# Kernel tuning notes

Measured on AMD Instinct MI355X. Metric: run time of the kernel, lower is better.

The kernel has to match this reference:

```python
import jax, jax.numpy as jnp
import numpy as np

MARGIN = 1.0
BATCH = 512
NFEAT = 128
NTRIP = 1024


def setup_inputs() -> dict:
    key = jax.random.key(0)
    k1, k2 = jax.random.split(key)
    embeddings = jax.random.normal(k1, (BATCH, NFEAT), dtype=jnp.float32)
    triplets = jax.random.randint(k2, (NTRIP, 3), 0, BATCH, dtype=jnp.int64)
    return {"embeddings": embeddings, "triplets": triplets}


def _triplet_loss(embeddings, triplets, margin):
    pivot = embeddings[triplets[:, 0]]
    positives = embeddings[triplets[:, 1]]
    negatives = embeddings[triplets[:, 2]]
    ap = jnp.sum((pivot - positives) ** 2, axis=1)
    an = jnp.sum((pivot - negatives) ** 2, axis=1)
    return jnp.mean(jax.nn.relu(ap - an + margin))


def _dist_corr_loss(embeddings):
    # embeddings: [B, n]; treat each feature column as a 1-D sample.
    B, n = embeddings.shape
    X = embeddings.T  # [n, B]
    # Per-column pairwise L1 distance matrices: [n, B, B]
    D = jnp.abs(X[:, :, None] - X[:, None, :])
    m = jnp.mean(D, axis=1)                      # [n, B] row/col means (D symmetric)
    g = jnp.mean(m, axis=1)                      # [n] grand means
    A = D - m[:, None, :] - m[:, :, None] + g[:, None, None]  # double-centered
    # S[i, j] = mean(A_i * A_j) over the B*B entries
    S = jnp.einsum('iab,jab->ij', A, A) / (B * B)
    diag = jnp.diagonal(S)                       # mean(A_i^2) = varA_i^2 pre-sqrt
    # dCov(i,j) = sqrt(S_ij); dCorr = dCov / sqrt(sqrt(S_ii)*sqrt(S_jj))
    denom = jnp.sqrt(jnp.sqrt(diag)[:, None] * jnp.sqrt(diag)[None, :])
    corr = jnp.sqrt(S) / denom                   # [n, n]
    iu, ju = jnp.triu_indices(n, k=1)
    return jnp.mean(corr[iu, ju])


def reference(embeddings, triplets):
    triplet_loss = _triplet_loss(embeddings, triplets, MARGIN)
    corr_loss = _dist_corr_loss(embeddings)
    return triplet_loss + corr_loss
```

## Files before the change

kernel.cpp:

```cpp
#include <hip/hip_runtime.h>
#include <hip/hip_bf16.h>

#define B_    512
#define F_    128
#define NTRIP 1024
#define MARGIN 1.0f
#define NBLK  32
#define NPAIRB 132
#define NFOLD  4
#define PREP  130

#define OFF_M    0
#define OFF_MT   65536
#define OFF_G    131072
#define OFF_TL   131200
#define OFF_SQ   131216
#define OFF_PART 147600

typedef __attribute__((ext_vector_type(8))) short bf16x8;
typedef __attribute__((ext_vector_type(4))) float f32x4;

#define LDS_ROW 20

__device__ inline unsigned int bf16r(float f) {
    unsigned int u = __float_as_uint(f);
    u += 0x7FFFu + ((u >> 16) & 1u);
    return u >> 16;
}

__global__ __launch_bounds__(512)
void k1_prep_pair(const float* __restrict__ emb, const int* __restrict__ trip,
                  float* __restrict__ m, float* __restrict__ mT,
                  float* __restrict__ g, float* __restrict__ tl,
                  float* __restrict__ sq, float* __restrict__ out,
                  unsigned short* __restrict__ part) {
    __shared__ __align__(16) unsigned int dt[4 * F_ * LDS_ROW];
    const int bid = blockIdx.x;
    const int t   = threadIdx.x;

    if (bid >= NPAIRB) {
        const int pbb = bid - NPAIRB;
        if (pbb < F_) {
            float*  x    = (float*)dt;
            float4* red4 = (float4*)((float*)dt + 512);
            const int i = pbb;
            if (i == 0 && t == 0) out[0] = 0.f;
            x[t] = emb[t * F_ + i];
            __syncthreads();
            const float xav = x[t];
            float s0 = 0.f, s1 = 0.f, s2 = 0.f, s3 = 0.f;
            for (int b = 0; b < B_; b += 4) {
                s0 += fabsf(xav - x[b]);
                s1 += fabsf(xav - x[b + 1]);
                s2 += fabsf(xav - x[b + 2]);
                s3 += fabsf(xav - x[b + 3]);
            }
            float s = (s0 + s1) + (s2 + s3);
            float mv = s * (1.f / B_);
            m[i * B_ + t]  = mv;
            mT[t * F_ + i] = mv;
            red4[t] = make_float4(s, xav, xav * xav, mv * mv);
            __syncthreads();
            for (int sh = 256; sh > 0; sh >>= 1) {
                if (t < sh) {
                    float4 a = red4[t], b = red4[t + sh];
                    red4[t] = make_float4(a.x + b.x, a.y + b.y, a.z + b.z, a.w + b.w);
                }
                __syncthreads();
            }
            if (t == 0) {
                float4 r = red4[0];
                const float Bf = (float)B_;
                float gi = r.x * (1.f / (Bf * Bf));
                g[i] = gi;
                float DD  = 2.f * Bf * r.z - 2.f * r.y * r.y;
                float Sii = DD * (1.f / (Bf * Bf)) - (2.f / Bf) * r.w + gi * gi;
                sq[i] = sqrtf(sqrtf(fmaxf(Sii, 0.f)));
            }
        } else {
            float* red = (float*)dt;
            const int tt = (pbb - F_) * 512 + t;
            int a = trip[3 * tt]     & (B_ - 1);
            int p = trip[3 * tt + 1] & (B_ - 1);
            int n = trip[3 * tt + 2] & (B_ - 1);
            const float4* ea = (const float4*)(emb + a * F_);
            const float4* ep = (const float4*)(emb + p * F_);
            const float4* en = (const float4*)(emb + n * F_);
            float ap = 0.f, an = 0.f;
            #pragma unroll 8
            for (int f4 = 0; f4 < F_ / 4; ++f4) {
                float4 va = ea[f4], vp = ep[f4], vn = en[f4];
                float d;
                d = va.x - vp.x; ap = fmaf(d, d, ap);
                d = va.y - vp.y; ap = fmaf(d, d, ap);
                d = va.z - vp.z; ap = fmaf(d, d, ap);
                d = va.w - vp.w; ap = fmaf(d, d, ap);
                d = va.x - vn.x; an = fmaf(d, d, an);
                d = va.y - vn.y; an = fmaf(d, d, an);
                d = va.z - vn.z; an = fmaf(d, d, an);
                d = va.w - vn.w; an = fmaf(d, d, an);
            }
            float l = fmaxf(ap - an + MARGIN, 0.f);
            red[t] = l;
            __syncthreads();
            for (int sh = 256; sh > 0; sh >>= 1) {
                if (t < sh) red[t] += red[t + sh];
                __syncthreads();
            }
            if (t == 0) tl[pbb - F_] = red[0];
        }
        return;
    }

    const int pbp = bid;
    const int lane = t & 63;
    const int w    = t >> 6;
    const int wr   = w >> 1;
    const int wc   = w & 1;
    const int i    = t & 127;
    const int pg   = t >> 7;
    const int fr_row = lane & 15;
    const int fr_k4  = (lane >> 4) * 4;

    int baA[NFOLD], bbA[NFOLD];
    #pragma unroll
    for (int u = 0; u < NFOLD; ++u) {
        int L = pbp + u * NPAIRB;
        int ba = 0, rem = L;
        while (rem >= NBLK - ba) { rem -= NBLK - ba; ++ba; }
        baA[u] = ba; bbA[u] = ba + rem;
    }

    f32x4 acc[2][4];
    #pragma unroll
    for (int q = 0; q < 2; ++q)
        #pragma unroll
        for (int c = 0; c < 4; ++c) acc[q][c] = (f32x4)(0.f);

    float xb[2][16], xa[2][4];
    #pragma unroll
    for (int b = 0; b < 16; ++b) xb[0][b] = emb[(bbA[0] * 16 + b) * F_ + i];
    #pragma unroll
    for (int k = 0; k < 4; ++k)
        xa[0][k] = emb[(baA[0] * 16 + (k >> 1) * 8 + pg * 2 + (k & 1)) * F_ + i];

    #pragma unroll
    for (int u = 0; u < NFOLD; ++u) {
        const int cu = u & 1, nx = cu ^ 1;
        const bool diag = (baA[u] == bbA[u]);
        #pragma unroll
        for (int h = 0; h < 2; ++h) {
            if (h | u) __syncthreads();
            #pragma unroll
            for (int ar2 = 0; ar2 < 2; ++ar2) {
                const float xav = xa[cu][h * 2 + ar2];
                const int pa = h * 8 + pg * 2 + ar2;
                unsigned int pk[8];
                #pragma unroll
                for (int q = 0; q < 8; ++q) {
                    float d0 = fabsf(xav - xb[cu][2 * q]);
                    float d1 = fabsf(xav - xb[cu][2 * q + 1]);
                    if (diag && pa >= 2 * q)     d0 = 0.f;
                    if (diag && pa >= 2 * q + 1) d1 = 0.f;
                    pk[q] = bf16r(d0) | (bf16r(d1) << 16);
                }
                unsigned int* dst = &dt[pg * (F_ * LDS_ROW) + i * LDS_ROW + ar2 * 8];
                *reinterpret_cast<uint4*>(dst)     = make_uint4(pk[0], pk[1], pk[2], pk[3]);
                *reinterpret_cast<uint4*>(dst + 4) = make_uint4(pk[4], pk[5], pk[6], pk[7]);
            }
            if (h == 1 && u < NFOLD - 1) {
                #pragma unroll
                for (int b = 0; b < 16; ++b)
                    xb[nx][b] = emb[(bbA[u + 1] * 16 + b) * F_ + i];
                #pragma unroll
                for (int k = 0; k < 4; ++k)
                    xa[nx][k] = emb[(baA[u + 1] * 16 + (k >> 1) * 8 + pg * 2 + (k & 1)) * F_ + i];
            }
            __syncthreads();
            #pragma unroll
            for (int c = 0; c < 4; ++c) {
                const unsigned int* base = &dt[c * (F_ * LDS_ROW)];
                const bf16x8 fA0 = *reinterpret_cast<const bf16x8*>(
                    &base[((wr * 2 + 0) * 16 + fr_row) * LDS_ROW + fr_k4]);
                const bf16x8 fA1 = *reinterpret_cast<const bf16x8*>(
                    &base[((wr * 2 + 1) * 16 + fr_row) * LDS_ROW + fr_k4]);
                #pragma unroll
                for (int cg = 0; cg < 4; ++cg) {
                    const bf16x8 fB = *reinterpret_cast<const bf16x8*>(
                        &base[((wc * 4 + cg) * 16 + fr_row) * LDS_ROW + fr_k4]);
                    acc[0][cg] = __builtin_amdgcn_mfma_f32_16x16x32_bf16(fA0, fB, acc[0][cg], 0, 0, 0);
                    acc[1][cg] = __builtin_amdgcn_mfma_f32_16x16x32_bf16(fA1, fB, acc[1][cg], 0, 0, 0);
                }
            }
        }
    }

    unsigned short* dstp = part + (size_t)pbp * (F_ * F_);
    const int cj = lane & 15;
    const int rsub = (lane >> 4) * 4;
    #pragma unroll
    for (int q = 0; q < 2; ++q)
        #pragma unroll
        for (int cg = 0; cg < 4; ++cg)
            #pragma unroll
            for (int r = 0; r < 4; ++r)
                dstp[((wr * 2 + q) * 16 + rsub + r) * F_ + (wc * 4 + cg) * 16 + cj] =
                    (unsigned short)bf16r(acc[q][cg][r]);
}

__global__ __launch_bounds__(512)
void k2_srow_final(const unsigned short* __restrict__ part,
                   const float* __restrict__ m, const float* __restrict__ mT,
                   const float* __restrict__ g, const float* __restrict__ sq,
                   const float* __restrict__ tl, float* __restrict__ out) {
    __shared__ float shT[16][64];
    __shared__ float shM[8][64];
    __shared__ float smi[B_];
    __shared__ float red[64];
    const int bid = blockIdx.x;
    const int i   = bid >> 1;
    const int jh  = bid & 1;
    const int t   = threadIdx.x;

    const int dw = t & 31;
    const int sl = t >> 5;
    const unsigned int* src = reinterpret_cast<const unsigned int*>(part)
                            + i * 64 + jh * 32 + dw;
    float tlo = 0.f, thi = 0.f;
    #pragma unroll
    for (int k = 0; k < 9; ++k) {
        const int s = sl + 16 * k;
        if (s < NPAIRB) {
            unsigned int v = src[(size_t)s * 8192];
            tlo += __uint_as_float(v << 16);
            thi += __uint_as_float(v & 0xFFFF0000u);
        }
    }
    shT[sl][dw * 2]     = tlo;
    shT[sl][dw * 2 + 1] = thi;
    smi[t] = m[i * B_ + t];
    __syncthreads();

    const int jl = t & 63;
    const int j  = jh * 64 + jl;
    const int q8 = t >> 6;
    float md = 0.f;
    const float* mta = mT + (size_t)(q8 * 64) * F_ + j;
    const float* mia = smi + q8 * 64;
    #pragma unroll 8
    for (int a = 0; a < 64; ++a) md = fmaf(mia[a], mta[(size_t)a * F_], md);
    shM[q8][jl] = md;
    __syncthreads();

    if (t < 64) {
        float T = 0.f;
        #pragma unroll
        for (int s = 0; s < 16; ++s) T += shT[s][t];
        float mdj = 0.f;
        #pragma unroll
        for (int s = 0; s < 8; ++s) mdj += shM[s][t];
        const int jj = jh * 64 + t;
        float Sij = 2.f * T * (1.f / ((float)B_ * (float)B_))
                  - (2.f / (float)B_) * mdj
                  + g[i] * g[jj];
        float c = 0.f;
        if (jj > i) c = sqrtf(fmaxf(Sij, 0.f)) / (sq[i] * sq[jj]);
        red[t] = c;
    }
    __syncthreads();
    for (int sh = 32; sh > 0; sh >>= 1) {
        if (t < sh) red[t] += red[t + sh];
        __syncthreads();
    }
    if (t == 0) {
        float v = red[0] * (1.f / 8128.f);
        if (bid == 0) v += (tl[0] + tl[1]) * (1.f / (float)NTRIP);
        atomicAdd(out, v);
    }
}

extern "C" void kernel_launch(void* const* d_in, const int* in_sizes, int n_in,
                              void* d_out, int out_size, void* d_ws, size_t ws_size,
                              hipStream_t stream) {
    const float* emb = (const float*)d_in[0];
    const int*   trp = (const int*)d_in[1];
    float* ws  = (float*)d_ws;
    float* m   = ws + OFF_M;
    float* mT  = ws + OFF_MT;
    float* g   = ws + OFF_G;
    float* tl  = ws + OFF_TL;
    float* sq  = ws + OFF_SQ;
    unsigned short* part = (unsigned short*)(ws + OFF_PART);
    float* out = (float*)d_out;

    k1_prep_pair  <<<NPAIRB + PREP, 512, 0, stream>>>(emb, trp, m, mT, g, tl, sq, out, part);
    k2_srow_final <<<256, 512, 0, stream>>>(part, m, mT, g, sq, tl, out);
}
```

Measured before the change: 39.33 us.

## Spread Gram pair blocks over 256 workgroups with 2–3 pairs each

The 528 block-pair tiles of the distance-matrix Gram product are now split across 256 workgroups: 240 handle 2 pairs and 16 handle 3. Previously 132 workgroups each handled 4 pairs. The goal is to fill more compute units on the GPU and shorten the longest per-workgroup chain. The register double-buffered prefetch of embedding values is removed, so global loads now happen inline with each step. The number of bf16 partial matrices grows, which increases partial-sum write traffic and the per-thread reduction loads in the final kernel.

```diff
diff --git a/kernel.cpp b/kernel.cpp
--- a/kernel.cpp
+++ b/kernel.cpp
@@ -6,8 +6,7 @@
 #define NTRIP 1024
 #define MARGIN 1.0f
 #define NBLK  32
-#define NPAIRB 132
-#define NFOLD  4
+#define NPAIRB 256
 #define PREP  130
 
 #define OFF_M    0
@@ -113,6 +112,9 @@
     }
 
     const int pbp = bid;
+    const int cnt  = (pbp >= 240) ? 3 : 2;
+    const int base = (pbp >= 240) ? 480 + (pbp - 240) * 3 : pbp * 2;
+
     const int lane = t & 63;
     const int w    = t >> 6;
     const int wr   = w >> 1;
@@ -122,44 +124,37 @@
     const int fr_row = lane & 15;
     const int fr_k4  = (lane >> 4) * 4;
 
-    int baA[NFOLD], bbA[NFOLD];
-    #pragma unroll
-    for (int u = 0; u < NFOLD; ++u) {
-        int L = pbp + u * NPAIRB;
-        int ba = 0, rem = L;
-        while (rem >= NBLK - ba) { rem -= NBLK - ba; ++ba; }
-        baA[u] = ba; bbA[u] = ba + rem;
-    }
-
     f32x4 acc[2][4];
     #pragma unroll
     for (int q = 0; q < 2; ++q)
         #pragma unroll
         for (int c = 0; c < 4; ++c) acc[q][c] = (f32x4)(0.f);
 
-    float xb[2][16], xa[2][4];
-    #pragma unroll
-    for (int b = 0; b < 16; ++b) xb[0][b] = emb[(bbA[0] * 16 + b) * F_ + i];
-    #pragma unroll
-    for (int k = 0; k < 4; ++k)
-        xa[0][k] = emb[(baA[0] * 16 + (k >> 1) * 8 + pg * 2 + (k & 1)) * F_ + i];
-
-    #pragma unroll
-    for (int u = 0; u < NFOLD; ++u) {
-        const int cu = u & 1, nx = cu ^ 1;
-        const bool diag = (baA[u] == bbA[u]);
+    for (int k = 0; k < cnt; ++k) {
+        const int L = base + k;
+        int ba = 0, rem = L;
+        while (rem >= NBLK - ba) { rem -= NBLK - ba; ++ba; }
+        const int bb = ba + rem;
+        const bool diag = (ba == bb);
+
+        float xb[16];
+        #pragma unroll
+        for (int b = 0; b < 16; ++b) xb[b] = emb[(bb * 16 + b) * F_ + i];
+
         #pragma unroll
         for (int h = 0; h < 2; ++h) {
-            if (h | u) __syncthreads();
+            const float xa0 = emb[(ba * 16 + h * 8 + pg * 2 + 0) * F_ + i];
+            const float xa1 = emb[(ba * 16 + h * 8 + pg * 2 + 1) * F_ + i];
+            if (k | h) __syncthreads();
             #pragma unroll
             for (int ar2 = 0; ar2 < 2; ++ar2) {
-                const float xav = xa[cu][h * 2 + ar2];
+                const float xav = ar2 ? xa1 : xa0;
                 const int pa = h * 8 + pg * 2 + ar2;
                 unsigned int pk[8];
                 #pragma unroll
                 for (int q = 0; q < 8; ++q) {
-                    float d0 = fabsf(xav - xb[cu][2 * q]);
-                    float d1 = fabsf(xav - xb[cu][2 * q + 1]);
+                    float d0 = fabsf(xav - xb[2 * q]);
+                    float d1 = fabsf(xav - xb[2 * q + 1]);
                     if (diag && pa >= 2 * q)     d0 = 0.f;
                     if (diag && pa >= 2 * q + 1) d1 = 0.f;
                     pk[q] = bf16r(d0) | (bf16r(d1) << 16);
@@ -168,26 +163,18 @@
                 *reinterpret_cast<uint4*>(dst)     = make_uint4(pk[0], pk[1], pk[2], pk[3]);
                 *reinterpret_cast<uint4*>(dst + 4) = make_uint4(pk[4], pk[5], pk[6], pk[7]);
             }
-            if (h == 1 && u < NFOLD - 1) {
-                #pragma unroll
-                for (int b = 0; b < 16; ++b)
-                    xb[nx][b] = emb[(bbA[u + 1] * 16 + b) * F_ + i];
-                #pragma unroll
-                for (int k = 0; k < 4; ++k)
-                    xa[nx][k] = emb[(baA[u + 1] * 16 + (k >> 1) * 8 + pg * 2 + (k & 1)) * F_ + i];
-            }
             __syncthreads();
             #pragma unroll
             for (int c = 0; c < 4; ++c) {
-                const unsigned int* base = &dt[c * (F_ * LDS_ROW)];
+                const unsigned int* cb = &dt[c * (F_ * LDS_ROW)];
                 const bf16x8 fA0 = *reinterpret_cast<const bf16x8*>(
-                    &base[((wr * 2 + 0) * 16 + fr_row) * LDS_ROW + fr_k4]);
+                    &cb[((wr * 2 + 0) * 16 + fr_row) * LDS_ROW + fr_k4]);
                 const bf16x8 fA1 = *reinterpret_cast<const bf16x8*>(
-                    &base[((wr * 2 + 1) * 16 + fr_row) * LDS_ROW + fr_k4]);
+                    &cb[((wr * 2 + 1) * 16 + fr_row) * LDS_ROW + fr_k4]);
                 #pragma unroll
                 for (int cg = 0; cg < 4; ++cg) {
                     const bf16x8 fB = *reinterpret_cast<const bf16x8*>(
-                        &base[((wc * 4 + cg) * 16 + fr_row) * LDS_ROW + fr_k4]);
+                        &cb[((wc * 4 + cg) * 16 + fr_row) * LDS_ROW + fr_k4]);
                     acc[0][cg] = __builtin_amdgcn_mfma_f32_16x16x32_bf16(fA0, fB, acc[0][cg], 0, 0, 0);
                     acc[1][cg] = __builtin_amdgcn_mfma_f32_16x16x32_bf16(fA1, fB, acc[1][cg], 0, 0, 0);
                 }
@@ -228,13 +215,10 @@
                             + i * 64 + jh * 32 + dw;
     float tlo = 0.f, thi = 0.f;
     #pragma unroll
-    for (int k = 0; k < 9; ++k) {
-        const int s = sl + 16 * k;
-        if (s < NPAIRB) {
-            unsigned int v = src[(size_t)s * 8192];
-            tlo += __uint_as_float(v << 16);
-            thi += __uint_as_float(v & 0xFFFF0000u);
-        }
+    for (int k = 0; k < 16; ++k) {
+        unsigned int v = src[(size_t)(sl + 16 * k) * 8192];
+        tlo += __uint_as_float(v << 16);
+        thi += __uint_as_float(v & 0xFFFF0000u);
     }
     shT[sl][dw * 2]     = tlo;
     shT[sl][dw * 2 + 1] = thi;
```

New measurement: 40.18 us. +2.2%, slower.
